# Optimization experiments

Measured on AMD Instinct MI355X. Metric: run time of the kernel, lower is better.

## Reference

```python
import jax, jax.numpy as jnp
import numpy as np

B, M, F_IN, DX, K, L, N_ALL = 8192, 10, 128, 128, 64, 32, 100000
NN = M - 1          # n_neigh
INF = float(M)


def layer_norm(x, g, b, eps=1e-5):
    mu = x.mean(-1, keepdims=True)
    var = ((x - mu) ** 2).mean(-1, keepdims=True)
    return (x - mu) * jax.lax.rsqrt(var + eps) * g + b


def bfs_dists(adj, mask):
    # normalized all-pairs hop distances via repeated boolean matmul (m=10 fixed)
    adj_bin = (adj > 1e-5).astype(jnp.float32)
    eye = jnp.eye(M, dtype=bool)
    d = jnp.where(eye[None], 0.0, jnp.where(adj_bin > 0, 1.0, INF))
    curr = adj_bin
    for k in range(2, M):
        curr = jnp.matmul(curr, adj_bin)
        d = jnp.where((curr > 0) & (d == INF), float(k), d)
    mask2 = mask[:, :, None] * mask[:, None, :]
    d = jnp.where(mask2 == 0, INF, d)
    return d / float(M)


def compute_sw(zb, zp, theta, vmask):
    # sliced Wasserstein-2 between batch point clouds [B,NN,d] and prototypes [K,NN,d]
    tn = theta / jnp.linalg.norm(theta, axis=1, keepdims=True)
    pb = jnp.einsum('bmd,ld->bml', zb, tn)
    pp = jnp.einsum('kmd,ld->kml', zp, tn)
    idx = jnp.argsort(pb, axis=1)
    pbs = jnp.take_along_axis(pb, idx, axis=1)
    pps = jnp.sort(pp, axis=1)
    w = jnp.take_along_axis(jnp.broadcast_to(vmask[:, :, None], pb.shape), idx, axis=1)
    w = w / (w.sum(axis=1, keepdims=True) + 1e-9)
    # sum_m w*(pb-pp)^2 expanded to avoid materializing [B,K,NN,L]
    t1 = (w * pbs ** 2).sum(axis=1)                   # [B,L]
    t2 = jnp.einsum('bml,kml->bkl', w * pbs, pps)     # [B,K,L]
    t3 = jnp.einsum('bml,kml->bkl', w, pps ** 2)
    return (t1[:, None, :] - 2.0 * t2 + t3).mean(axis=-1)


def compute_radial(rb, rp, vmask):
    idx = jnp.argsort(rb, axis=1)
    rbs = jnp.take_along_axis(rb, idx, axis=1)
    rps = jnp.sort(rp, axis=1)
    w = jnp.take_along_axis(vmask, idx, axis=1)
    w = w / (w.sum(axis=1, keepdims=True) + 1e-9)
    return (((rbs[:, None, :] - rps[None]) ** 2) * w[:, None, :]).sum(-1)


def setup_inputs() -> dict:
    key = jax.random.key(0)
    ks = jax.random.split(key, 16)
    up = (jax.random.uniform(ks[0], (B, M, M)) < 0.3).astype(jnp.float32)
    adj = jnp.maximum(up, up.transpose(0, 2, 1)) * (1.0 - jnp.eye(M))
    features = jax.random.normal(ks[1], (N_ALL, F_IN), jnp.float32)
    idxs = jax.random.randint(ks[2], (B, M), 0, N_ALL + 1)   # N_ALL == padding index
    rn = lambda k, s, sc=0.02: sc * jax.random.normal(k, s, jnp.float32)
    params = dict(
        x_lin_w=rn(ks[3], (F_IN, DX), 0.05), x_lin_b=jnp.zeros((DX,)),
        x_ln_g=jnp.ones((DX,)), x_ln_b=jnp.zeros((DX,)),
        s_ln_g=jnp.ones((NN,)), s_ln_b=jnp.zeros((NN,)),
        theta_x=jax.random.normal(ks[4], (L, DX), jnp.float32),
        theta_s=jax.random.normal(ks[5], (L, NN), jnp.float32),
        alpha_raw=jnp.zeros(()),
        an_w1=rn(ks[6], (DX, 32), 0.1), an_b1=jnp.zeros((32,)),
        an_w2=rn(ks[7], (32, 1), 0.1), an_b2=jnp.zeros((1,)),
        wn_w1=rn(ks[8], (2 * DX, 32), 0.1), wn_b1=jnp.zeros((32,)),
        wn_w2=rn(ks[9], (32, 1), 0.1), wn_b2=jnp.zeros((1,)),
        w_raw=jnp.zeros(()),
        proto_root=jax.random.normal(ks[10], (K, F_IN), jnp.float32),
        proto_neigh=jax.random.normal(ks[11], (K, NN, F_IN), jnp.float32),
        proto_rad=jax.random.uniform(ks[12], (K, NN)),
        proto_dn=jax.random.uniform(ks[13], (NN * (NN - 1) // 2, K), minval=-0.5, maxval=0.5),
        log_gamma=jnp.asarray(np.log(0.01), jnp.float32),
    )
    return {"adj": adj, "features": features, "idxs": idxs, **params}


def reference(adj, features, idxs, x_lin_w, x_lin_b, x_ln_g, x_ln_b, s_ln_g, s_ln_b,
              theta_x, theta_s, alpha_raw, an_w1, an_b1, an_w2, an_b2,
              wn_w1, wn_b1, wn_w2, wn_b2, w_raw,
              proto_root, proto_neigh, proto_rad, proto_dn, log_gamma):
    b = adj.shape[0]
    x_all = jnp.concatenate([features, jnp.zeros((1, F_IN), features.dtype)], 0)
    x_patch = x_all[idxs]                             # [B,M,F]
    x_root, x_neigh = x_patch[:, 0], x_patch[:, 1:]
    vmask = (idxs[:, 1:] != N_ALL).astype(jnp.float32)   # [B,NN]
    lin = lambda x: x @ x_lin_w + x_lin_b
    h_root = layer_norm(lin(x_root), x_ln_g, x_ln_b)
    h_proto_root = layer_norm(lin(proto_root), x_ln_g, x_ln_b)
    d_root_feat = (jnp.sum(h_root ** 2, -1)[:, None] + jnp.sum(h_proto_root ** 2, -1)[None]
                   - 2.0 * h_root @ h_proto_root.T)   # squared cdist [B,K]
    full_mask = jnp.concatenate([jnp.ones((b, 1), jnp.float32), vmask], 1)
    dists_full = bfs_dists(adj, full_mask)
    d_radial_str = compute_radial(dists_full[:, 0, 1:], proto_rad, vmask)
    h_neigh = layer_norm(lin(x_neigh), x_ln_g, x_ln_b)     # dropout = identity (eval)
    h_proto_neigh = layer_norm(lin(proto_neigh), x_ln_g, x_ln_b)
    sw_neigh_feat = compute_sw(h_neigh, h_proto_neigh, theta_x, vmask)
    hs_neigh = layer_norm(jnp.sort(dists_full[:, 1:, 1:], axis=1), s_ln_g, s_ln_b)
    ti, tj = np.triu_indices(NN, 1)
    C = jnp.zeros((K, NN, NN)).at[:, ti, tj].set(jax.nn.sigmoid(proto_dn).T)
    C = C + C.transpose(0, 2, 1)
    hs_proto = layer_norm(jnp.sort(C, axis=1), s_ln_g, s_ln_b)
    sw_neigh_str = compute_sw(hs_neigh, hs_proto, theta_s, vmask)
    h_pooled = (h_neigh * vmask[:, :, None]).sum(1) / (vmask.sum(1, keepdims=True) + 1e-9)
    alpha_logit = jnp.maximum(h_pooled @ an_w1 + an_b1, 0.0) @ an_w2 + an_b2   # [B,1]
    alpha = jax.nn.sigmoid(alpha_raw + alpha_logit)
    # pairwise w_net([h_root; h_proto_root]) without materializing [B,K,2*DX]
    hb = h_root @ wn_w1[:DX] + wn_b1                   # [B,32]
    hp = h_proto_root @ wn_w1[DX:]                     # [K,32]
    w_logit = (jnp.maximum(hb[:, None] + hp[None], 0.0) @ wn_w2)[..., 0] + wn_b2[0]
    w = jax.nn.sigmoid(w_raw + w_logit)                # [B,K]
    d_feat = w * d_root_feat + (1.0 - w) * sw_neigh_feat
    d_str = w * d_radial_str + (1.0 - w) * sw_neigh_str
    d_fgw = alpha * d_feat + (1.0 - alpha) * d_str
    return jnp.exp(-jnp.exp(log_gamma) * d_fgw)        # [B,K]
```

## Files before the change

### kernel.cpp

```cpp
#include <hip/hip_runtime.h>
#include <hip/hip_bf16.h>

typedef unsigned short u16;
typedef __attribute__((ext_vector_type(8))) short short8;
typedef __attribute__((ext_vector_type(4))) float f32x4;

#define NN 9
#define DX 128
#define KP 64
#define LL 32
#define NALL 100000
#define NBM 16
#define HXR 136
#define HXB (10 * HXR)

#define MFMA(a, b, c) __builtin_amdgcn_mfma_f32_16x16x32_bf16(a, b, c, 0, 0, 0)
#define WFENCE() __threadfence_block()

__device__ __align__(16) float g_tns[LL * NN];
__device__ __align__(16) float g_hprn[KP];
__device__ __align__(16) float g_hpt[32 * KP];
__device__ __align__(16) float g_rpst[NN * KP];
__device__ __align__(16) u16   g_pW[16384];
__device__ __align__(16) u16   g_pBt[4096];
__device__ __align__(16) u16   g_pBr[8192];
__device__ __align__(16) u16   g_pBx[36864];
__device__ __align__(16) u16   g_pBs[36864];
__device__ __align__(16) u16   g_pAn[4096];
__device__ __align__(16) u16   g_pWn[4096];

__device__ __forceinline__ float bf2f(u16 u) {
    union { unsigned u; float f; } v; v.u = ((unsigned)u) << 16; return v.f;
}
__device__ __forceinline__ u16 f2bf(float f) {
    __hip_bfloat16 h = __float2bfloat16(f);
    union { __hip_bfloat16 h; u16 u; } v; v.h = h; return v.u;
}
__device__ __forceinline__ float ldv(const void* p, long i, int f32) {
    return f32 ? ((const float*)p)[i] : bf2f(((const u16*)p)[i]);
}
__device__ __forceinline__ float sigmoidf(float x) { return 1.f / (1.f + expf(-x)); }

__device__ __forceinline__ int bfrag_idx(int ksteps, int ncol, int kd) {
    int ntile = ncol >> 4, n = ncol & 15;
    int kstep = kd >> 5, quad = (kd >> 3) & 3, j = kd & 7;
    return ((ntile * ksteps + kstep) * 64 + quad * 16 + n) * 8 + j;
}

__device__ __forceinline__ void rank9(const float* v, int* r) {
#pragma unroll
    for (int m = 0; m < 9; m++) {
        int rk = 0;
#pragma unroll
        for (int n = 0; n < 9; n++)
            rk += (v[n] < v[m]) || (v[n] == v[m] && n < m);
        r[m] = rk;
    }
}

__global__ __launch_bounds__(256) void k_pack(
    const void* xlw, const void* theta_x, const void* theta_s,
    const void* an_w1, const void* wn_w1, const void* xlg) {
    int t = threadIdx.x;
    const int f32 = (((const u16*)xlg)[0] == 0);
    if (blockIdx.x == 0) {
        for (int i = t; i < 16384; i += 256) {
            int c = i >> 7, d = i & 127;
            g_pW[bfrag_idx(4, d, c)] = f2bf(ldv(xlw, i, f32));
        }
    } else if (blockIdx.x == 1) {
        if (t < 32) {
            float s = 0;
            for (int d = 0; d < 128; d++) { float v = ldv(theta_x, t * 128 + d, f32); s = fmaf(v, v, s); }
            float inv = 1.f / sqrtf(s);
            for (int d = 0; d < 128; d++)
                g_pBt[bfrag_idx(4, t, d)] = f2bf(ldv(theta_x, t * 128 + d, f32) * inv);
        } else if (t < 64) {
            int l = t - 32;
            float s = 0;
            for (int j = 0; j < 9; j++) { float v = ldv(theta_s, l * 9 + j, f32); s = fmaf(v, v, s); }
            float inv = 1.f / sqrtf(s);
            for (int j = 0; j < 9; j++) g_tns[l * 9 + j] = ldv(theta_s, l * 9 + j, f32) * inv;
        }
    } else {
        for (int i = t; i < 4096; i += 256) {
            int d = i >> 5, j = i & 31;
            g_pAn[bfrag_idx(4, j, d)] = f2bf(ldv(an_w1, i, f32));
            g_pWn[bfrag_idx(4, j, d)] = f2bf(ldv(wn_w1, i, f32));
        }
    }
}

__global__ __launch_bounds__(256, 4) void k_proto(
    const void* proto_root, const void* proto_neigh,
    const void* xlb, const void* xlg, const void* xlbt,
    const void* slg, const void* slb, const void* wn_w1,
    const void* proto_rad, const void* proto_dn) {
    __shared__ __align__(16) u16   WfL[16384];
    __shared__ __align__(16) u16   hXpb[1280];
    __shared__ __align__(16) float pbX[288];
    __shared__ __align__(16) float Cm[84];
    __shared__ __align__(16) float hsnP[84];

    int t = threadIdx.x, lane = t & 63, w = t >> 6;
    const int f32 = (((const u16*)xlg)[0] == 0);
    int fm = lane & 15, quad = lane >> 4;
    int kb = blockIdx.x;

    {
        const short8* src = (const short8*)g_pW;
        short8* dst = (short8*)WfL;
#pragma unroll
        for (int i = 0; i < 8; i++) dst[t + 256 * i] = src[t + 256 * i];
    }

    int lr = w * 16 + fm;
    const void* abuf = proto_root; long aoff = 0;
    bool arow = (lr < 10);
    if (arow) {
        if (lr < 9) { abuf = proto_neigh; aoff = (long)(kb * 9 + lr) * 128; }
        else        { abuf = proto_root;  aoff = (long)kb * 128; }
    }
    short8 af[4];
#pragma unroll
    for (int ks = 0; ks < 4; ks++) af[ks] = (short8){0, 0, 0, 0, 0, 0, 0, 0};
    if (arow) {
        if (f32) {
#pragma unroll
            for (int ks = 0; ks < 4; ks++) {
                const f32x4* src = (const f32x4*)((const float*)abuf + aoff + ks * 32 + quad * 8);
                f32x4 v0 = src[0], v1 = src[1];
                u16* ap = (u16*)&af[ks];
#pragma unroll
                for (int j = 0; j < 4; j++) { ap[j] = f2bf(v0[j]); ap[4 + j] = f2bf(v1[j]); }
            }
        } else {
#pragma unroll
            for (int ks = 0; ks < 4; ks++)
                af[ks] = *(const short8*)((const u16*)abuf + aoff + ks * 32 + quad * 8);
        }
    }
    float bias8[8], gg8[8], bb8[8];
#pragma unroll
    for (int nt = 0; nt < 8; nt++) {
        int col = nt * 16 + fm;
        bias8[nt] = ldv(xlb, col, f32);
        gg8[nt]   = ldv(xlg, col, f32);
        bb8[nt]   = ldv(xlbt, col, f32);
    }
    __syncthreads();

    if (w == 0) {
        f32x4 acc[8];
#pragma unroll
        for (int nt = 0; nt < 8; nt++) acc[nt] = (f32x4){0.f, 0.f, 0.f, 0.f};
#pragma unroll
        for (int ks = 0; ks < 4; ks++) {
#pragma unroll
            for (int nt = 0; nt < 8; nt++) {
                short8 bf = *(const short8*)(WfL + ((nt * 4 + ks) * 64 + lane) * 8);
                acc[nt] = MFMA(af[ks], bf, acc[nt]);
            }
        }
#pragma unroll
        for (int reg = 0; reg < 4; reg++) {
            float s = 0, q = 0;
#pragma unroll
            for (int nt = 0; nt < 8; nt++) {
                float v = acc[nt][reg] + bias8[nt];
                s += v; q = fmaf(v, v, q);
            }
#pragma unroll
            for (int m = 1; m < 16; m <<= 1) { s += __shfl_xor(s, m); q += __shfl_xor(q, m); }
            float mu = s * (1.f / 128.f);
            float var = fmaxf(q * (1.f / 128.f) - mu * mu, 0.f);
            float rs = rsqrtf(var + 1e-5f);
            int rowD = quad * 4 + reg;
            if (rowD < 10) {
#pragma unroll
                for (int nt = 0; nt < 8; nt++) {
                    float val = (acc[nt][reg] + bias8[nt] - mu) * rs * gg8[nt] + bb8[nt];
                    hXpb[rowD * 128 + nt * 16 + fm] = f2bf(val);
                }
            }
        }
    }
    __syncthreads();

    for (int i = t; i < 128; i += 256)
        g_pBr[bfrag_idx(4, kb, i)] = hXpb[1152 + i];
    if (w == 0) {
        float v0 = bf2f(hXpb[1152 + lane]);
        float v1 = bf2f(hXpb[1216 + lane]);
        float q = v0 * v0 + v1 * v1;
#pragma unroll
        for (int m = 32; m >= 1; m >>= 1) q += __shfl_xor(q, m);
        if (lane == 0) g_hprn[kb] = q;
    }
    {
        int j = t >> 3, sub = t & 7;
        float a = 0;
#pragma unroll
        for (int dd = 0; dd < 16; dd++) {
            int d = sub * 16 + dd;
            a = fmaf(bf2f(hXpb[1152 + d]), ldv(wn_w1, (128 + d) * 32 + j, f32), a);
        }
        a += __shfl_xor(a, 1);
        a += __shfl_xor(a, 2);
        a += __shfl_xor(a, 4);
        if (sub == 0) g_hpt[j * 64 + kb] = a;
    }
    if (t == 0) {
        float v[9]; int r[9];
#pragma unroll
        for (int m = 0; m < 9; m++) v[m] = ldv(proto_rad, kb * 9 + m, f32);
        rank9(v, r);
#pragma unroll
        for (int m = 0; m < 9; m++) g_rpst[r[m] * 64 + kb] = v[m];
    }
    if (w == 0) {
        f32x4 acc0 = {0.f, 0.f, 0.f, 0.f}, acc1 = {0.f, 0.f, 0.f, 0.f};
        const u16* arow2 = hXpb + fm * 128;
#pragma unroll
        for (int ks = 0; ks < 4; ks++) {
            short8 afp = {0, 0, 0, 0, 0, 0, 0, 0};
            if (fm < 9) afp = *(const short8*)(arow2 + ks * 32 + quad * 8);
            short8 b0 = *(const short8*)(g_pBt + ((0 * 4 + ks) * 64 + lane) * 8);
            short8 b1 = *(const short8*)(g_pBt + ((1 * 4 + ks) * 64 + lane) * 8);
            acc0 = MFMA(afp, b0, acc0);
            acc1 = MFMA(afp, b1, acc1);
        }
#pragma unroll
        for (int reg = 0; reg < 4; reg++) {
            int row = quad * 4 + reg;
            if (row < 9) {
                pbX[row * 32 + fm]      = acc0[reg];
                pbX[row * 32 + 16 + fm] = acc1[reg];
            }
        }
    }
    for (int i = t; i < 81; i += 256) {
        int ii = i / 9, jj = i % 9; float v = 0.f;
        if (ii != jj) {
            int a = (ii < jj) ? ii : jj, b2 = (ii < jj) ? jj : ii;
            int p = a * 8 - a * (a - 1) / 2 + (b2 - a - 1);
            v = sigmoidf(ldv(proto_dn, p * 64 + kb, f32));
        }
        Cm[i] = v;
    }
    __syncthreads();
    if (t < 32) {
// ... 30 lines not shown
        float rs = rsqrtf(var + 1e-5f);
#pragma unroll
        for (int j = 0; j < 9; j++)
            hsnP[t * 9 + j] = (Cm[t * 9 + j] - mu) * rs * ldv(slg, j, f32) + ldv(slb, j, f32);
    }
    __syncthreads();
    if (t < 32) {
#pragma unroll
        for (int m = 0; m < 9; m++) {
            float a = 0;
#pragma unroll
            for (int j = 0; j < 9; j++) a = fmaf(hsnP[m * 9 + j], g_tns[t * 9 + j], a);
            pbX[m * 32 + t] = a;
        }
    }
    __syncthreads();
    if (t < 32) {
        float v[9]; int r[9];
#pragma unroll
        for (int m = 0; m < 9; m++) v[m] = pbX[m * 32 + t];
        rank9(v, r);
#pragma unroll
        for (int m = 0; m < 9; m++) {
            int kd = t * 9 + r[m];
            g_pBs[bfrag_idx(18, kb, kd)]       = f2bf(v[m] * v[m]);
            g_pBs[bfrag_idx(18, kb, 288 + kd)] = f2bf(v[m]);
        }
    }
}

struct M3 {
    u16   Cf[NBM][584];
    u16   Cs[NBM][584];
    u16   hpoolb[NBM][136];
    u16   hX[NBM][HXB];
    float pb[NBM][288];
    float df[NBM][100];
    float hst[NBM][81];
    float drad[NBM][65];
    float hbv[NBM][33];
    float rbss[NBM][9], wrad[NBM][9];
    float sc[NBM][9];
};
__global__ __launch_bounds__(1024, 4) void k_main(
    const void* adj, const void* feat, const int* idxs,
    const void* slg, const void* slb,
    const void* xlb, const void* xlg, const void* xlbt,
    const void* an_b1, const void* an_w2, const void* an_b2,
    const void* wn_b1, const void* wn_w2, const void* wn_b2,
    const void* alpha_raw, const void* w_raw, const void* log_gamma,
    void* out, int B) {
    __shared__ __align__(16) M3 S;
    int t = threadIdx.x, lane = t & 63, w = t >> 6;
    const int f32 = (((const u16*)xlg)[0] == 0);
    int fm = lane & 15, quad = lane >> 4;
    int bw = blockIdx.x * NBM + w;
    bool bv = (bw < B);

    unsigned long long mb = 0; float nv = 1e-9f, inv = 0.f;

    if (bv) {
        bool azero = true; long aoff = 0;
        if (fm < 10) {
            int id = idxs[bw * 10 + fm];
            if (id != NALL) { azero = false; aoff = (long)id * 128; }
        }
        short8 af[4];
#pragma unroll
        for (int ks = 0; ks < 4; ks++) af[ks] = (short8){0, 0, 0, 0, 0, 0, 0, 0};
        if (!azero) {
            if (f32) {
#pragma unroll
                for (int ks = 0; ks < 4; ks++) {
                    const f32x4* src = (const f32x4*)((const float*)feat + aoff + ks * 32 + quad * 8);
                    f32x4 v0 = src[0], v1 = src[1];
                    u16* ap = (u16*)&af[ks];
#pragma unroll
                    for (int j = 0; j < 4; j++) { ap[j] = f2bf(v0[j]); ap[4 + j] = f2bf(v1[j]); }
                }
            } else {
#pragma unroll
                for (int ks = 0; ks < 4; ks++)
                    af[ks] = *(const short8*)((const u16*)feat + aoff + ks * 32 + quad * 8);
            }
        }

        bool valid = false;
        if (lane < 10) {
            int id = idxs[bw * 10 + lane];
            valid = (lane == 0) || (id != NALL);
        }
        mb = __ballot(valid);
        nv = (float)__popcll(mb & 0x3FEull) + 1e-9f;
        inv = 1.f / nv;
        unsigned rowbits = 0;
        if (lane < 10) {
            for (int j = 0; j < 10; j++)
                if (ldv(adj, (long)bw * 100 + lane * 10 + j, f32) > 1e-5f) rowbits |= 1u << j;
        }
        int dl[10];
#pragma unroll
        for (int j = 0; j < 10; j++) dl[j] = (j == lane) ? 0 : (((rowbits >> j) & 1) ? 1 : 10);
        unsigned reach = (lane < 10) ? (rowbits | (1u << lane)) : 0u;
        for (int s = 2; s <= 9; s++) {
            unsigned nr = reach;
#pragma unroll
            for (int j = 0; j < 10; j++) {
                unsigned rj = __shfl(rowbits, j);
                if ((reach >> j) & 1) nr |= rj;
            }
            unsigned add = nr & ~reach;
#pragma unroll
            for (int j = 0; j < 10; j++) if ((add >> j) & 1) dl[j] = s;
            reach = nr;
            if (__all(add == 0)) break;
        }
        if (lane < 10) {
            int mi = (int)((mb >> lane) & 1);
#pragma unroll
            for (int j = 0; j < 10; j++) {
                int mj = (int)((mb >> j) & 1);
                S.df[w][lane * 10 + j] = (mi && mj) ? (float)dl[j] * 0.1f : 1.0f;
            }
        }
        {
            float v[9];
#pragma unroll
            for (int m = 0; m < 9; m++) {
                float vm = ((mb >> (1 + m)) & 1) ? (float)dl[1 + m] * 0.1f : 1.0f;
                v[m] = __shfl(vm, 0);
            }
            if (lane < 9) {
                float mine = v[0];
#pragma unroll
                for (int m = 1; m < 9; m++) if (lane == m) mine = v[m];
                int rk = 0;
#pragma unroll
                for (int n = 0; n < 9; n++) rk += (v[n] < mine) || (v[n] == mine && n < lane);
                S.rbss[w][rk] = mine;
                S.wrad[w][rk] = (((mb >> (1 + lane)) & 1) ? 1.f : 0.f) * inv;
            }
        }

        {
            float bias8[8], gg8[8], bb8[8];
#pragma unroll
            for (int nt = 0; nt < 8; nt++) {
                int col = nt * 16 + fm;
                bias8[nt] = ldv(xlb, col, f32);
                gg8[nt]   = ldv(xlg, col, f32);
                bb8[nt]   = ldv(xlbt, col, f32);
            }
            f32x4 acc[8];
#pragma unroll
            for (int nt = 0; nt < 8; nt++) acc[nt] = (f32x4){0.f, 0.f, 0.f, 0.f};
#pragma unroll
            for (int ks = 0; ks < 4; ks++) {
#pragma unroll
                for (int nt = 0; nt < 8; nt++) {
                    short8 bf = *(const short8*)(g_pW + ((nt * 4 + ks) * 64 + lane) * 8);
                    acc[nt] = MFMA(af[ks], bf, acc[nt]);
                }
            }
#pragma unroll
            for (int reg = 0; reg < 4; reg++) {
                float s = 0, q = 0;
#pragma unroll
                for (int nt = 0; nt < 8; nt++) {
                    float v = acc[nt][reg] + bias8[nt];
                    s += v; q = fmaf(v, v, q);
                }
#pragma unroll
                for (int m = 1; m < 16; m <<= 1) { s += __shfl_xor(s, m); q += __shfl_xor(q, m); }
                float mu = s * (1.f / 128.f);
                float var = fmaxf(q * (1.f / 128.f) - mu * mu, 0.f);
                float rs = rsqrtf(var + 1e-5f);
                int rowD = quad * 4 + reg;
                if (rowD < 10) {
#pragma unroll
                    for (int nt = 0; nt < 8; nt++) {
                        float val = (acc[nt][reg] + bias8[nt] - mu) * rs * gg8[nt] + bb8[nt];
                        S.hX[w][rowD * HXR + nt * 16 + fm] = f2bf(val);
                    }
                }
            }
        }
        WFENCE();

        {
            float v0 = bf2f(S.hX[w][lane]), v1 = bf2f(S.hX[w][64 + lane]);
            float q = v0 * v0 + v1 * v1;
#pragma unroll
            for (int m = 32; m >= 1; m >>= 1) q += __shfl_xor(q, m);
            if (lane == 0) S.sc[w][1] = q;
        }
        for (int dd = lane; dd < 128; dd += 64) {
            float a = 0;
#pragma unroll
            for (int m = 0; m < 9; m++) {
                float hv = bf2f(S.hX[w][(1 + m) * HXR + dd]);
                float msk = ((mb >> (1 + m)) & 1) ? 1.f : 0.f;
                a = fmaf(hv, msk, a);
            }
            S.hpoolb[w][dd] = f2bf(a * inv);
        }
        {
            f32x4 acc0 = {0.f, 0.f, 0.f, 0.f}, acc1 = {0.f, 0.f, 0.f, 0.f};
            const u16* arow = S.hX[w] + (1 + fm) * HXR;
#pragma unroll
            for (int ks = 0; ks < 4; ks++) {
                short8 afn = {0, 0, 0, 0, 0, 0, 0, 0};
                if (fm < 9) afn = *(const short8*)(arow + ks * 32 + quad * 8);
                short8 b0 = *(const short8*)(g_pBt + ((0 * 4 + ks) * 64 + lane) * 8);
                short8 b1 = *(const short8*)(g_pBt + ((1 * 4 + ks) * 64 + lane) * 8);
                acc0 = MFMA(afn, b0, acc0);
                acc1 = MFMA(afn, b1, acc1);
            }
#pragma unroll
            for (int reg = 0; reg < 4; reg++) {
                int row = quad * 4 + reg;
                if (row < 9) {
                    S.pb[w][row * 32 + fm]      = acc0[reg];
                    S.pb[w][row * 32 + 16 + fm] = acc1[reg];
                }
            }
        }
        WFENCE();

        {
            float t1 = 0;
            if (lane < 32) {
                float v[9]; int r[9];
#pragma unroll
                for (int m = 0; m < 9; m++) v[m] = S.pb[w][m * 32 + lane];
                rank9(v, r);
#pragma unroll
                for (int m = 0; m < 9; m++) {
                    float wgt = (((mb >> (1 + m)) & 1) ? 1.f : 0.f) * inv;
                    int slot = lane * 9 + r[m];
                    S.Cf[w][slot]       = f2bf(wgt);
                    S.Cf[w][288 + slot] = f2bf(-2.f * wgt * v[m]);
                    t1 = fmaf(wgt * v[m], v[m], t1);
                }
            }
#pragma unroll
            for (int m = 16; m >= 1; m >>= 1) t1 += __shfl_xor(t1, m);
            if (lane == 0) S.sc[w][3] = t1;
        }
        if (lane < 9) {
            float v[9]; int r[9];
#pragma unroll
            for (int i = 0; i < 9; i++) v[i] = S.df[w][(1 + i) * 10 + 1 + lane];
            rank9(v, r);
#pragma unroll
            for (int i = 0; i < 9; i++) S.hst[w][r[i] * 9 + lane] = v[i];
        }
        {
            float acc = 0;
#pragma unroll
            for (int m = 0; m < 9; m++) {
                float d0 = S.rbss[w][m] - g_rpst[m * 64 + lane];
                acc = fmaf(d0 * d0, S.wrad[w][m], acc);
            }
            S.drad[w][lane] = acc;
        }
        WFENCE();

        if (lane < 9) {
            float vv[9];
#pragma unroll
            for (int j = 0; j < 9; j++) vv[j] = S.hst[w][lane * 9 + j];
            float mu = 0;
#pragma unroll
            for (int j = 0; j < 9; j++) mu += vv[j];
            mu *= (1.f / 9.f);
            float var = 0;
#pragma unroll
            for (int j = 0; j < 9; j++) { float d0 = vv[j] - mu; var = fmaf(d0, d0, var); }
            var *= (1.f / 9.f);
            float rs = rsqrtf(var + 1e-5f);
#pragma unroll
            for (int j = 0; j < 9; j++)
                S.hst[w][lane * 9 + j] = (vv[j] - mu) * rs * ldv(slg, j, f32) + ldv(slb, j, f32);
        }
        WFENCE();

        {
            int l = lane & 31;
            int m0 = (lane < 32) ? 0 : 5, m1 = (lane < 32) ? 5 : 9;
            for (int m = m0; m < m1; m++) {
                float a = 0;
#pragma unroll
                for (int j = 0; j < 9; j++) a = fmaf(S.hst[w][m * 9 + j], g_tns[l * 9 + j], a);
                S.pb[w][m * 32 + l] = a;
            }
        }
        WFENCE();

        {
            float t1 = 0;
            if (lane < 32) {
                float v[9]; int r[9];
#pragma unroll
                for (int m = 0; m < 9; m++) v[m] = S.pb[w][m * 32 + lane];
                rank9(v, r);
#pragma unroll
                for (int m = 0; m < 9; m++) {
                    float wgt = (((mb >> (1 + m)) & 1) ? 1.f : 0.f) * inv;
                    int slot = lane * 9 + r[m];
                    S.Cs[w][slot]       = f2bf(wgt);
                    S.Cs[w][288 + slot] = f2bf(-2.f * wgt * v[m]);
                    t1 = fmaf(wgt * v[m], v[m], t1);
                }
            }
#pragma unroll
            for (int m = 16; m >= 1; m >>= 1) t1 += __shfl_xor(t1, m);
            if (lane == 0) S.sc[w][4] = t1;
        }
    }
    __syncthreads();

    f32x4 rd = {0.f, 0.f, 0.f, 0.f};
    f32x4 accF = {0.f, 0.f, 0.f, 0.f}, accS = {0.f, 0.f, 0.f, 0.f};
    if (w < 4) {
#pragma unroll
        for (int ks = 0; ks < 4; ks++) {
            short8 af = {0, 0, 0, 0, 0, 0, 0, 0};
            if (blockIdx.x * NBM + fm < B)
                af = *(const short8*)(S.hX[fm] + ks * 32 + quad * 8);
            short8 bfr = *(const short8*)(g_pBr + ((w * 4 + ks) * 64 + lane) * 8);
            rd = MFMA(af, bfr, rd);
        }
#pragma unroll
        for (int ks = 0; ks < 18; ks++) {
            short8 aF = *(const short8*)(S.Cf[fm] + ks * 32 + quad * 8);
            short8 aS = *(const short8*)(S.Cs[fm] + ks * 32 + quad * 8);
            short8 bF = *(const short8*)(g_pBx + ((w * 18 + ks) * 64 + lane) * 8);
            short8 bS = *(const short8*)(g_pBs + ((w * 18 + ks) * 64 + lane) * 8);
            accF = MFMA(aF, bF, accF);
            accS = MFMA(aS, bS, accS);
        }
    } else if (w == 4) {
        f32x4 a0 = {0.f, 0.f, 0.f, 0.f}, a1 = {0.f, 0.f, 0.f, 0.f};
#pragma unroll
        for (int ks = 0; ks < 4; ks++) {
            short8 af = {0, 0, 0, 0, 0, 0, 0, 0};
            if (blockIdx.x * NBM + fm < B)
                af = *(const short8*)(S.hX[fm] + ks * 32 + quad * 8);
            short8 b0 = *(const short8*)(g_pWn + ((0 * 4 + ks) * 64 + lane) * 8);
            short8 b1 = *(const short8*)(g_pWn + ((1 * 4 + ks) * 64 + lane) * 8);
            a0 = MFMA(af, b0, a0);
            a1 = MFMA(af, b1, a1);
        }
        float wb0 = ldv(wn_b1, fm, f32), wb1 = ldv(wn_b1, 16 + fm, f32);
#pragma unroll
        for (int reg = 0; reg < 4; reg++) {
            int b = quad * 4 + reg;
            S.hbv[b][fm]      = a0[reg] + wb0;
            S.hbv[b][16 + fm] = a1[reg] + wb1;
        }
    } else if (w == 5) {
        f32x4 a0 = {0.f, 0.f, 0.f, 0.f}, a1 = {0.f, 0.f, 0.f, 0.f};
#pragma unroll
        for (int ks = 0; ks < 4; ks++) {
            short8 af = *(const short8*)(S.hpoolb[fm] + ks * 32 + quad * 8);
            short8 b0 = *(const short8*)(g_pAn + ((0 * 4 + ks) * 64 + lane) * 8);
            short8 b1 = *(const short8*)(g_pAn + ((1 * 4 + ks) * 64 + lane) * 8);
            a0 = MFMA(af, b0, a0);
            a1 = MFMA(af, b1, a1);
        }
        float ab0 = ldv(an_b1, fm, f32), ab1 = ldv(an_b1, 16 + fm, f32);
        float aw0 = ldv(an_w2, fm, f32), aw1 = ldv(an_w2, 16 + fm, f32);
        float araw = ldv(alpha_raw, 0, f32), ab2 = ldv(an_b2, 0, f32);
#pragma unroll
        for (int reg = 0; reg < 4; reg++) {
            float s = fmaxf(a0[reg] + ab0, 0.f) * aw0 + fmaxf(a1[reg] + ab1, 0.f) * aw1;
            s += __shfl_xor(s, 1); s += __shfl_xor(s, 2);
            s += __shfl_xor(s, 4); s += __shfl_xor(s, 8);
            if (fm == 0) S.sc[quad * 4 + reg][2] = sigmoidf(araw + s + ab2);
        }
    }
// ... 34 lines not shown
    }
}

extern "C" void kernel_launch(void* const* d_in, const int* in_sizes, int n_in,
                              void* d_out, int out_size, void* d_ws, size_t ws_size,
                              hipStream_t stream) {
    const void* adj  = d_in[0];
    const void* feat = d_in[1];
    const int*  idxs = (const int*)d_in[2];
    const void* xlw  = d_in[3];
    const void* xlb  = d_in[4];
    const void* xlg  = d_in[5];
    const void* xlbt = d_in[6];
    const void* slg  = d_in[7];
    const void* slb  = d_in[8];
    const void* thx  = d_in[9];
    const void* ths  = d_in[10];
    const void* araw = d_in[11];
    const void* anw1 = d_in[12];
    const void* anb1 = d_in[13];
    const void* anw2 = d_in[14];
    const void* anb2 = d_in[15];
    const void* wnw1 = d_in[16];
    const void* wnb1 = d_in[17];
    const void* wnw2 = d_in[18];
    const void* wnb2 = d_in[19];
    const void* wraw = d_in[20];
    const void* prt  = d_in[21];
    const void* prn  = d_in[22];
    const void* prad = d_in[23];
    const void* pdn  = d_in[24];
    const void* lgam = d_in[25];
    int B = in_sizes[2] / 10;

    k_pack<<<3, 256, 0, stream>>>(xlw, thx, ths, anw1, wnw1, xlg);
    k_proto<<<KP, 256, 0, stream>>>(prt, prn, xlb, xlg, xlbt, slg, slb, wnw1,
                                    prad, pdn);
    k_main<<<(B + NBM - 1) / NBM, 1024, 0, stream>>>(adj, feat, idxs, slg, slb,
                                  xlb, xlg, xlbt,
                                  anb1, anw2, anb2, wnb1, wnw2, wnb2,
                                  araw, wraw, lgam, d_out, B);
}
```

Baseline: 226.8 us.

## Split per-sample preprocessing into separate kernel merged with prototype blocks

Moves the per-sample work (feature gather, linear+layernorm, BFS distances, projections, sorting, radial distances) out of the 1024-thread main kernel into a new 256-thread kernel with one wave per sample. The new kernel shares its grid with the prototype blocks. Results are staged through global scratch buffers, which the main kernel then loads into shared memory before its MFMA distance stage. This aims for higher occupancy and overlap of the serial per-sample work with prototype processing. The cost is extra global traffic for the intermediate buffers and reading the weight fragments from global instead of LDS.

```diff
diff --git a/kernel.cpp b/kernel.cpp
--- a/kernel.cpp
+++ b/kernel.cpp
@@ -10,9 +10,11 @@
 #define KP 64
 #define LL 32
 #define NALL 100000
+#define BMAX 8192
 #define NBM 16
+#define NBP 64
 #define HXR 136
-#define HXB (10 * HXR)
+#define WSTR 4736
 
 #define MFMA(a, b, c) __builtin_amdgcn_mfma_f32_16x16x32_bf16(a, b, c, 0, 0, 0)
 #define WFENCE() __threadfence_block()
@@ -21,6 +23,14 @@
 __device__ __align__(16) float g_hprn[KP];
 __device__ __align__(16) float g_hpt[32 * KP];
 __device__ __align__(16) float g_rpst[NN * KP];
+__device__ __align__(16) u16   g_hroot[BMAX * DX];
+__device__ __align__(16) u16   g_hpool[BMAX * DX];
+__device__ __align__(16) float g_hrn[BMAX];
+__device__ __align__(16) u16   g_Cf[BMAX * 576];
+__device__ __align__(16) u16   g_Cs[BMAX * 576];
+__device__ __align__(16) float g_drad[BMAX * 64];
+__device__ __align__(16) float g_t1x[BMAX];
+__device__ __align__(16) float g_t1s[BMAX];
 __device__ __align__(16) u16   g_pW[16384];
 __device__ __align__(16) u16   g_pBt[4096];
 __device__ __align__(16) u16   g_pBr[8192];
@@ -60,7 +70,7 @@
 
 __global__ __launch_bounds__(256) void k_pack(
     const void* xlw, const void* theta_x, const void* theta_s,
-    const void* an_w1, const void* wn_w1, const void* xlg) {
+    const void* an_w1, const void* wn_w1, const void* proto_rad, const void* xlg) {
     int t = threadIdx.x;
     const int f32 = (((const u16*)xlg)[0] == 0);
     if (blockIdx.x == 0) {
@@ -81,6 +91,14 @@
             for (int j = 0; j < 9; j++) { float v = ldv(theta_s, l * 9 + j, f32); s = fmaf(v, v, s); }
             float inv = 1.f / sqrtf(s);
             for (int j = 0; j < 9; j++) g_tns[l * 9 + j] = ldv(theta_s, l * 9 + j, f32) * inv;
+        } else if (t < 128) {
+            int k = t - 64;
+            float v[9]; int r[9];
+#pragma unroll
+            for (int m = 0; m < 9; m++) v[m] = ldv(proto_rad, k * 9 + m, f32);
+            rank9(v, r);
+#pragma unroll
+            for (int m = 0; m < 9; m++) g_rpst[r[m] * 64 + k] = v[m];
         }
     } else {
         for (int i = t; i < 4096; i += 256) {
@@ -91,66 +109,330 @@
     }
 }
 
-__global__ __launch_bounds__(256, 4) void k_proto(
+__global__ __launch_bounds__(256, 5) void k_lin(
+    const void* adj, const void* feat, const int* idxs,
     const void* proto_root, const void* proto_neigh,
     const void* xlb, const void* xlg, const void* xlbt,
     const void* slg, const void* slb, const void* wn_w1,
-    const void* proto_rad, const void* proto_dn) {
-    __shared__ __align__(16) u16   WfL[16384];
-    __shared__ __align__(16) u16   hXpb[1280];
-    __shared__ __align__(16) float pbX[288];
-    __shared__ __align__(16) float Cm[84];
-    __shared__ __align__(16) float hsnP[84];
+    const void* proto_dn, int B) {
+    __shared__ __align__(16) char sm[4 * WSTR];
 
     int t = threadIdx.x, lane = t & 63, w = t >> 6;
     const int f32 = (((const u16*)xlg)[0] == 0);
     int fm = lane & 15, quad = lane >> 4;
+    bool isProto = (blockIdx.x < (unsigned)NBP);
+
+    if (!isProto) {
+        u16*   hSw = (u16*)(sm + w * WSTR);
+        float* pbw = (float*)(sm + w * WSTR + 2720);
+        float* dfw = (float*)(sm + w * WSTR + 3872);
+        float* stw = (float*)(sm + w * WSTR + 4272);
+        float* rbw = (float*)(sm + w * WSTR + 4608);
+        float* wrw = (float*)(sm + w * WSTR + 4644);
+
+        int bw = (blockIdx.x - NBP) * 4 + w;
+        if (bw >= B) return;
+
+        bool valid = false;
+        if (lane < 10) {
+            int id = idxs[bw * 10 + lane];
+            valid = (lane == 0) || (id != NALL);
+        }
+        unsigned long long mb = __ballot(valid);
+        float inv = 1.f / ((float)__popcll(mb & 0x3FEull) + 1e-9f);
+
+        bool azero = true; long aoff = 0;
+        if (fm < 10) {
+            int id2 = idxs[bw * 10 + fm];
+            if (id2 != NALL) { azero = false; aoff = (long)id2 * 128; }
+        }
+        short8 af[4];
+#pragma unroll
+        for (int ks = 0; ks < 4; ks++) af[ks] = (short8){0, 0, 0, 0, 0, 0, 0, 0};
+        if (!azero) {
+            if (f32) {
+#pragma unroll
+                for (int ks = 0; ks < 4; ks++) {
+                    const f32x4* src = (const f32x4*)((const float*)feat + aoff + ks * 32 + quad * 8);
+                    f32x4 v0 = src[0], v1 = src[1];
+                    u16* ap = (u16*)&af[ks];
+#pragma unroll
+                    for (int j = 0; j < 4; j++) { ap[j] = f2bf(v0[j]); ap[4 + j] = f2bf(v1[j]); }
+                }
+            } else {
+#pragma unroll
+                for (int ks = 0; ks < 4; ks++)
+                    af[ks] = *(const short8*)((const u16*)feat + aoff + ks * 32 + quad * 8);
+            }
+        }
+
+        unsigned rowbits = 0;
+        if (lane < 10) {
+            for (int j = 0; j < 10; j++)
+                if (ldv(adj, (long)bw * 100 + lane * 10 + j, f32) > 1e-5f) rowbits |= 1u << j;
+        }
+        int dl[10];
+#pragma unroll
+        for (int j = 0; j < 10; j++) dl[j] = (j == lane) ? 0 : (((rowbits >> j) & 1) ? 1 : 10);
+        unsigned reach = (lane < 10) ? (rowbits | (1u << lane)) : 0u;
+        for (int s = 2; s <= 9; s++) {
+            unsigned nr = reach;
+#pragma unroll
+            for (int j = 0; j < 10; j++) {
+                unsigned rj = __shfl(rowbits, j);
+                if ((reach >> j) & 1) nr |= rj;
+            }
+            unsigned add = nr & ~reach;
+#pragma unroll
+            for (int j = 0; j < 10; j++) if ((add >> j) & 1) dl[j] = s;
+            reach = nr;
+            if (__all(add == 0)) break;
+        }
+        if (lane < 10) {
+            int mi = (int)((mb >> lane) & 1);
+#pragma unroll
+            for (int j = 0; j < 10; j++) {
+                int mj = (int)((mb >> j) & 1);
+                dfw[lane * 10 + j] = (mi && mj) ? (float)dl[j] * 0.1f : 1.0f;
+            }
+        }
+        {
+            float v[9];
+#pragma unroll
+            for (int m = 0; m < 9; m++) {
+                float vm = ((mb >> (1 + m)) & 1) ? (float)dl[1 + m] * 0.1f : 1.0f;
+                v[m] = __shfl(vm, 0);
+            }
+            if (lane < 9) {
+                float mine = v[0];
+#pragma unroll
+                for (int m = 1; m < 9; m++) if (lane == m) mine = v[m];
+                int rk = 0;
+#pragma unroll
+                for (int n = 0; n < 9; n++) rk += (v[n] < mine) || (v[n] == mine && n < lane);
+                rbw[rk] = mine;
+                wrw[rk] = (((mb >> (1 + lane)) & 1) ? 1.f : 0.f) * inv;
+            }
+        }
+
+        {
+            float bias8[8], gg8[8], bb8[8];
+#pragma unroll
+            for (int nt = 0; nt < 8; nt++) {
+                int col = nt * 16 + fm;
+                bias8[nt] = ldv(xlb, col, f32);
+                gg8[nt]   = ldv(xlg, col, f32);
+                bb8[nt]   = ldv(xlbt, col, f32);
+            }
+            f32x4 acc[8];
+#pragma unroll
+            for (int nt = 0; nt < 8; nt++) acc[nt] = (f32x4){0.f, 0.f, 0.f, 0.f};
+#pragma unroll
+            for (int ks = 0; ks < 4; ks++) {
+#pragma unroll
+                for (int nt = 0; nt < 8; nt++) {
+                    short8 bf = *(const short8*)(g_pW + ((nt * 4 + ks) * 64 + lane) * 8);
+                    acc[nt] = MFMA(af[ks], bf, acc[nt]);
+                }
+            }
+#pragma unroll
+            for (int reg = 0; reg < 4; reg++) {
+                float s = 0, q = 0;
+#pragma unroll
+                for (int nt = 0; nt < 8; nt++) {
+                    float v = acc[nt][reg] + bias8[nt];
+                    s += v; q = fmaf(v, v, q);
+                }
+#pragma unroll
+                for (int m = 1; m < 16; m <<= 1) { s += __shfl_xor(s, m); q += __shfl_xor(q, m); }
+                float mu = s * (1.f / 128.f);
+                float var = fmaxf(q * (1.f / 128.f) - mu * mu, 0.f);
+                float rs = rsqrtf(var + 1e-5f);
+                int rowD = quad * 4 + reg;
+                if (rowD < 10) {
+#pragma unroll
+                    for (int nt = 0; nt < 8; nt++) {
+                        float val = (acc[nt][reg] + bias8[nt] - mu) * rs * gg8[nt] + bb8[nt];
+                        hSw[rowD * HXR + nt * 16 + fm] = f2bf(val);
+                    }
+                }
+            }
+        }
+        WFENCE();
+
+        if (lane < 16)
+            ((short8*)(g_hroot + (long)bw * 128))[lane] = ((const short8*)hSw)[lane];
+        {
+            float v0 = bf2f(hSw[lane]), v1 = bf2f(hSw[64 + lane]);
+            float q = v0 * v0 + v1 * v1;
+#pragma unroll
+            for (int m = 32; m >= 1; m >>= 1) q += __shfl_xor(q, m);
+            if (lane == 0) g_hrn[bw] = q;
+        }
+        {
+            float a0 = 0, a1 = 0;
+            int c0 = lane * 2, c1 = lane * 2 + 1;
+#pragma unroll
+            for (int m = 0; m < 9; m++) {
+                float msk = ((mb >> (1 + m)) & 1) ? 1.f : 0.f;
+                a0 = fmaf(bf2f(hSw[(1 + m) * HXR + c0]), msk, a0);
+                a1 = fmaf(bf2f(hSw[(1 + m) * HXR + c1]), msk, a1);
+            }
+            unsigned pk = (unsigned)f2bf(a0 * inv) | ((unsigned)f2bf(a1 * inv) << 16);
+            ((unsigned*)(g_hpool + (long)bw * 128))[lane] = pk;
+        }
+
+        {
+            f32x4 acc0 = {0.f, 0.f, 0.f, 0.f}, acc1 = {0.f, 0.f, 0.f, 0.f};
+            const u16* arow = hSw + (1 + fm) * HXR;
+#pragma unroll
+            for (int ks = 0; ks < 4; ks++) {
+                short8 afn = {0, 0, 0, 0, 0, 0, 0, 0};
+                if (fm < 9) afn = *(const short8*)(arow + ks * 32 + quad * 8);
+                short8 b0 = *(const short8*)(g_pBt + ((0 * 4 + ks) * 64 + lane) * 8);
+                short8 b1 = *(const short8*)(g_pBt + ((1 * 4 + ks) * 64 + lane) * 8);
+                acc0 = MFMA(afn, b0, acc0);
+                acc1 = MFMA(afn, b1, acc1);
+            }
+#pragma unroll
+            for (int reg = 0; reg < 4; reg++) {
+                int row = quad * 4 + reg;
+                if (row < 9) {
+                    pbw[row * 32 + fm]      = acc0[reg];
+                    pbw[row * 32 + 16 + fm] = acc1[reg];
+                }
+            }
+        }
+        WFENCE();
+
+        {
+            float t1 = 0;
+            if (lane < 32) {
+                float v[9]; int r[9];
+#pragma unroll
+                for (int m = 0; m < 9; m++) v[m] = pbw[m * 32 + lane];
+                rank9(v, r);
+#pragma unroll
+                for (int m = 0; m < 9; m++) {
+                    float wgt = (((mb >> (1 + m)) & 1) ? 1.f : 0.f) * inv;
+                    int slot = lane * 9 + r[m];
+                    g_Cf[(long)bw * 576 + slot]       = f2bf(wgt);
+                    g_Cf[(long)bw * 576 + 288 + slot] = f2bf(-2.f * wgt * v[m]);
+                    t1 = fmaf(wgt * v[m], v[m], t1);
+                }
+            }
+#pragma unroll
+            for (int m = 16; m >= 1; m >>= 1) t1 += __shfl_xor(t1, m);
+            if (lane == 0) g_t1x[bw] = t1;
+        }
+        if (lane < 9) {
+            float v[9]; int r[9];
+#pragma unroll
+            for (int i = 0; i < 9; i++) v[i] = dfw[(1 + i) * 10 + 1 + lane];
+            rank9(v, r);
+#pragma unroll
+            for (int i = 0; i < 9; i++) stw[r[i] * 9 + lane] = v[i];
+        }
+        WFENCE();
+        if (lane < 9) {
+            float vv[9];
+#pragma unroll
+            for (int j = 0; j < 9; j++) vv[j] = stw[lane * 9 + j];
+            float mu = 0;
+#pragma unroll
+            for (int j = 0; j < 9; j++) mu += vv[j];
+            mu *= (1.f / 9.f);
+            float var = 0;
+#pragma unroll
+            for (int j = 0; j < 9; j++) { float d0 = vv[j] - mu; var = fmaf(d0, d0, var); }
+            var *= (1.f / 9.f);
+            float rs = rsqrtf(var + 1e-5f);
+#pragma unroll
+            for (int j = 0; j < 9; j++)
+                stw[lane * 9 + j] = (vv[j] - mu) * rs * ldv(slg, j, f32) + ldv(slb, j, f32);
+        }
+        WFENCE();
+        {
+            int l = lane & 31;
+            int m0 = (lane < 32) ? 0 : 5, m1 = (lane < 32) ? 5 : 9;
+            for (int m = m0; m < m1; m++) {
+                float a = 0;
+#pragma unroll
+                for (int j = 0; j < 9; j++) a = fmaf(stw[m * 9 + j], g_tns[l * 9 + j], a);
+                pbw[m * 32 + l] = a;
+            }
+        }
+        WFENCE();
+        {
+            float t1 = 0;
+            if (lane < 32) {
+                float v[9]; int r[9];
+#pragma unroll
+                for (int m = 0; m < 9; m++) v[m] = pbw[m * 32 + lane];
+                rank9(v, r);
+#pragma unroll
+                for (int m = 0; m < 9; m++) {
+                    float wgt = (((mb >> (1 + m)) & 1) ? 1.f : 0.f) * inv;
+                    int slot = lane * 9 + r[m];
+                    g_Cs[(long)bw * 576 + slot]       = f2bf(wgt);
+                    g_Cs[(long)bw * 576 + 288 + slot] = f2bf(-2.f * wgt * v[m]);
+                    t1 = fmaf(wgt * v[m], v[m], t1);
+                }
+            }
+#pragma unroll
+            for (int m = 16; m >= 1; m >>= 1) t1 += __shfl_xor(t1, m);
+            if (lane == 0) g_t1s[bw] = t1;
+        }
+        {
+            float a = 0;
+#pragma unroll
+            for (int m = 0; m < 9; m++) {
+                float d0 = rbw[m] - g_rpst[m * 64 + lane];
+                a = fmaf(d0 * d0, wrw[m], a);
+            }
+            g_drad[(long)bw * 64 + lane] = a;
+        }
+        return;
+    }
+
+    u16*   hXpb = (u16*)sm;
+    float* pbX  = (float*)(sm + 2560);
+    float* Cm   = (float*)(sm + 3712);
+    float* hsnP = (float*)(sm + 4048);
     int kb = blockIdx.x;
 
-    {
-        const short8* src = (const short8*)g_pW;
-        short8* dst = (short8*)WfL;
-#pragma unroll
-        for (int i = 0; i < 8; i++) dst[t + 256 * i] = src[t + 256 * i];
-    }
-
-    int lr = w * 16 + fm;
-    const void* abuf = proto_root; long aoff = 0;
-    bool arow = (lr < 10);
-    if (arow) {
-        if (lr < 9) { abuf = proto_neigh; aoff = (long)(kb * 9 + lr) * 128; }
+    if (w == 0) {
+        const void* abuf; long aoff;
+        if (fm < 9) { abuf = proto_neigh; aoff = (long)(kb * 9 + fm) * 128; }
         else        { abuf = proto_root;  aoff = (long)kb * 128; }
-    }
-    short8 af[4];
-#pragma unroll
-    for (int ks = 0; ks < 4; ks++) af[ks] = (short8){0, 0, 0, 0, 0, 0, 0, 0};
-    if (arow) {
-        if (f32) {
-#pragma unroll
-            for (int ks = 0; ks < 4; ks++) {
-                const f32x4* src = (const f32x4*)((const float*)abuf + aoff + ks * 32 + quad * 8);
-                f32x4 v0 = src[0], v1 = src[1];
-                u16* ap = (u16*)&af[ks];
-#pragma unroll
-                for (int j = 0; j < 4; j++) { ap[j] = f2bf(v0[j]); ap[4 + j] = f2bf(v1[j]); }
-            }
-        } else {
-#pragma unroll
-            for (int ks = 0; ks < 4; ks++)
-                af[ks] = *(const short8*)((const u16*)abuf + aoff + ks * 32 + quad * 8);
-        }
-    }
-    float bias8[8], gg8[8], bb8[8];
-#pragma unroll
-    for (int nt = 0; nt < 8; nt++) {
-        int col = nt * 16 + fm;
-        bias8[nt] = ldv(xlb, col, f32);
-        gg8[nt]   = ldv(xlg, col, f32);
-        bb8[nt]   = ldv(xlbt, col, f32);
-    }
-    __syncthreads();
-
-    if (w == 0) {
+        bool arow = (fm < 10);
+        short8 af[4];
+#pragma unroll
+        for (int ks = 0; ks < 4; ks++) af[ks] = (short8){0, 0, 0, 0, 0, 0, 0, 0};
+        if (arow) {
+            if (f32) {
+#pragma unroll
+                for (int ks = 0; ks < 4; ks++) {
+                    const f32x4* src = (const f32x4*)((const float*)abuf + aoff + ks * 32 + quad * 8);
+                    f32x4 v0 = src[0], v1 = src[1];
+                    u16* ap = (u16*)&af[ks];
+#pragma unroll
+                    for (int j = 0; j < 4; j++) { ap[j] = f2bf(v0[j]); ap[4 + j] = f2bf(v1[j]); }
+                }
+            } else {
+#pragma unroll
+                for (int ks = 0; ks < 4; ks++)
+                    af[ks] = *(const short8*)((const u16*)abuf + aoff + ks * 32 + quad * 8);
+            }
+        }
+        float bias8[8], gg8[8], bb8[8];
+#pragma unroll
+        for (int nt = 0; nt < 8; nt++) {
+            int col = nt * 16 + fm;
+            bias8[nt] = ldv(xlb, col, f32);
+            gg8[nt]   = ldv(xlg, col, f32);
+            bb8[nt]   = ldv(xlbt, col, f32);
+        }
         f32x4 acc[8];
 #pragma unroll
         for (int nt = 0; nt < 8; nt++) acc[nt] = (f32x4){0.f, 0.f, 0.f, 0.f};
@@ -158,7 +440,7 @@
         for (int ks = 0; ks < 4; ks++) {
 #pragma unroll
             for (int nt = 0; nt < 8; nt++) {
-                short8 bf = *(const short8*)(WfL + ((nt * 4 + ks) * 64 + lane) * 8);
+                short8 bf = *(const short8*)(g_pW + ((nt * 4 + ks) * 64 + lane) * 8);
                 acc[nt] = MFMA(af[ks], bf, acc[nt]);
             }
         }
@@ -209,14 +491,6 @@
         a += __shfl_xor(a, 2);
         a += __shfl_xor(a, 4);
         if (sub == 0) g_hpt[j * 64 + kb] = a;
-    }
-    if (t == 0) {
-        float v[9]; int r[9];
-#pragma unroll
-        for (int m = 0; m < 9; m++) v[m] = ldv(proto_rad, kb * 9 + m, f32);
-        rank9(v, r);
-#pragma unroll
-        for (int m = 0; m < 9; m++) g_rpst[r[m] * 64 + kb] = v[m];
     }
     if (w == 0) {
         f32x4 acc0 = {0.f, 0.f, 0.f, 0.f}, acc1 = {0.f, 0.f, 0.f, 0.f};
@@ -313,24 +587,17 @@
 struct M3 {
     u16   Cf[NBM][584];
     u16   Cs[NBM][584];
+    u16   hrootL[NBM][136];
     u16   hpoolb[NBM][136];
-    u16   hX[NBM][HXB];
-    float pb[NBM][288];
-    float df[NBM][100];
-    float hst[NBM][81];
     float drad[NBM][65];
     float hbv[NBM][33];
-    float rbss[NBM][9], wrad[NBM][9];
     float sc[NBM][9];
 };
-__global__ __launch_bounds__(1024, 4) void k_main(
-    const void* adj, const void* feat, const int* idxs,
-    const void* slg, const void* slb,
-    const void* xlb, const void* xlg, const void* xlbt,
+__global__ __launch_bounds__(1024, 8) void k_main(
     const void* an_b1, const void* an_w2, const void* an_b2,
     const void* wn_b1, const void* wn_w2, const void* wn_b2,
     const void* alpha_raw, const void* w_raw, const void* log_gamma,
-    void* out, int B) {
+    const void* xlg, void* out, int B) {
     __shared__ __align__(16) M3 S;
     int t = threadIdx.x, lane = t & 63, w = t >> 6;
     const int f32 = (((const u16*)xlg)[0] == 0);
@@ -338,265 +605,36 @@
     int bw = blockIdx.x * NBM + w;
     bool bv = (bw < B);
 
-    unsigned long long mb = 0; float nv = 1e-9f, inv = 0.f;
-
     if (bv) {
-        bool azero = true; long aoff = 0;
-        if (fm < 10) {
-            int id = idxs[bw * 10 + fm];
-            if (id != NALL) { azero = false; aoff = (long)id * 128; }
-        }
-        short8 af[4];
-#pragma unroll
-        for (int ks = 0; ks < 4; ks++) af[ks] = (short8){0, 0, 0, 0, 0, 0, 0, 0};
-        if (!azero) {
-            if (f32) {
-#pragma unroll
-                for (int ks = 0; ks < 4; ks++) {
-                    const f32x4* src = (const f32x4*)((const float*)feat + aoff + ks * 32 + quad * 8);
-                    f32x4 v0 = src[0], v1 = src[1];
-                    u16* ap = (u16*)&af[ks];
-#pragma unroll
-                    for (int j = 0; j < 4; j++) { ap[j] = f2bf(v0[j]); ap[4 + j] = f2bf(v1[j]); }
-                }
-            } else {
-#pragma unroll
-                for (int ks = 0; ks < 4; ks++)
-                    af[ks] = *(const short8*)((const u16*)feat + aoff + ks * 32 + quad * 8);
-            }
-        }
-
-        bool valid = false;
-        if (lane < 10) {
-            int id = idxs[bw * 10 + lane];
-            valid = (lane == 0) || (id != NALL);
-        }
-        mb = __ballot(valid);
-        nv = (float)__popcll(mb & 0x3FEull) + 1e-9f;
-        inv = 1.f / nv;
-        unsigned rowbits = 0;
-        if (lane < 10) {
-            for (int j = 0; j < 10; j++)
-                if (ldv(adj, (long)bw * 100 + lane * 10 + j, f32) > 1e-5f) rowbits |= 1u << j;
-        }
-        int dl[10];
-#pragma unroll
-        for (int j = 0; j < 10; j++) dl[j] = (j == lane) ? 0 : (((rowbits >> j) & 1) ? 1 : 10);
-        unsigned reach = (lane < 10) ? (rowbits | (1u << lane)) : 0u;
-        for (int s = 2; s <= 9; s++) {
-            unsigned nr = reach;
-#pragma unroll
-            for (int j = 0; j < 10; j++) {
-                unsigned rj = __shfl(rowbits, j);
-                if ((reach >> j) & 1) nr |= rj;
-            }
-            unsigned add = nr & ~reach;
-#pragma unroll
-            for (int j = 0; j < 10; j++) if ((add >> j) & 1) dl[j] = s;
-            reach = nr;
-            if (__all(add == 0)) break;
-        }
-        if (lane < 10) {
-            int mi = (int)((mb >> lane) & 1);
-#pragma unroll
-            for (int j = 0; j < 10; j++) {
-                int mj = (int)((mb >> j) & 1);
-                S.df[w][lane * 10 + j] = (mi && mj) ? (float)dl[j] * 0.1f : 1.0f;
-            }
-        }
-        {
-            float v[9];
-#pragma unroll
-            for (int m = 0; m < 9; m++) {
-                float vm = ((mb >> (1 + m)) & 1) ? (float)dl[1 + m] * 0.1f : 1.0f;
-                v[m] = __shfl(vm, 0);
-            }
-            if (lane < 9) {
-                float mine = v[0];
-#pragma unroll
-                for (int m = 1; m < 9; m++) if (lane == m) mine = v[m];
-                int rk = 0;
-#pragma unroll
-                for (int n = 0; n < 9; n++) rk += (v[n] < mine) || (v[n] == mine && n < lane);
-                S.rbss[w][rk] = mine;
-                S.wrad[w][rk] = (((mb >> (1 + lane)) & 1) ? 1.f : 0.f) * inv;
-            }
-        }
-
-        {
-            float bias8[8], gg8[8], bb8[8];
-#pragma unroll
-            for (int nt = 0; nt < 8; nt++) {
-                int col = nt * 16 + fm;
-                bias8[nt] = ldv(xlb, col, f32);
-                gg8[nt]   = ldv(xlg, col, f32);
-                bb8[nt]   = ldv(xlbt, col, f32);
-            }
-            f32x4 acc[8];
-#pragma unroll
-            for (int nt = 0; nt < 8; nt++) acc[nt] = (f32x4){0.f, 0.f, 0.f, 0.f};
-#pragma unroll
-            for (int ks = 0; ks < 4; ks++) {
-#pragma unroll
-                for (int nt = 0; nt < 8; nt++) {
-                    short8 bf = *(const short8*)(g_pW + ((nt * 4 + ks) * 64 + lane) * 8);
-                    acc[nt] = MFMA(af[ks], bf, acc[nt]);
-                }
-            }
-#pragma unroll
-            for (int reg = 0; reg < 4; reg++) {
-                float s = 0, q = 0;
-#pragma unroll
-                for (int nt = 0; nt < 8; nt++) {
-                    float v = acc[nt][reg] + bias8[nt];
-                    s += v; q = fmaf(v, v, q);
-                }
-#pragma unroll
-                for (int m = 1; m < 16; m <<= 1) { s += __shfl_xor(s, m); q += __shfl_xor(q, m); }
-                float mu = s * (1.f / 128.f);
-                float var = fmaxf(q * (1.f / 128.f) - mu * mu, 0.f);
-                float rs = rsqrtf(var + 1e-5f);
-                int rowD = quad * 4 + reg;
-                if (rowD < 10) {
-#pragma unroll
-                    for (int nt = 0; nt < 8; nt++) {
-                        float val = (acc[nt][reg] + bias8[nt] - mu) * rs * gg8[nt] + bb8[nt];
-                        S.hX[w][rowD * HXR + nt * 16 + fm] = f2bf(val);
-                    }
-                }
-            }
-        }
-        WFENCE();
-
-        {
-            float v0 = bf2f(S.hX[w][lane]), v1 = bf2f(S.hX[w][64 + lane]);
-            float q = v0 * v0 + v1 * v1;
-#pragma unroll
-            for (int m = 32; m >= 1; m >>= 1) q += __shfl_xor(q, m);
-            if (lane == 0) S.sc[w][1] = q;
-        }
-        for (int dd = lane; dd < 128; dd += 64) {
-            float a = 0;
-#pragma unroll
-            for (int m = 0; m < 9; m++) {
-                float hv = bf2f(S.hX[w][(1 + m) * HXR + dd]);
-                float msk = ((mb >> (1 + m)) & 1) ? 1.f : 0.f;
-                a = fmaf(hv, msk, a);
-            }
-            S.hpoolb[w][dd] = f2bf(a * inv);
-        }
-        {
-            f32x4 acc0 = {0.f, 0.f, 0.f, 0.f}, acc1 = {0.f, 0.f, 0.f, 0.f};
-            const u16* arow = S.hX[w] + (1 + fm) * HXR;
-#pragma unroll
-            for (int ks = 0; ks < 4; ks++) {
-                short8 afn = {0, 0, 0, 0, 0, 0, 0, 0};
-                if (fm < 9) afn = *(const short8*)(arow + ks * 32 + quad * 8);
-                short8 b0 = *(const short8*)(g_pBt + ((0 * 4 + ks) * 64 + lane) * 8);
-                short8 b1 = *(const short8*)(g_pBt + ((1 * 4 + ks) * 64 + lane) * 8);
-                acc0 = MFMA(afn, b0, acc0);
-                acc1 = MFMA(afn, b1, acc1);
-            }
-#pragma unroll
-            for (int reg = 0; reg < 4; reg++) {
-                int row = quad * 4 + reg;
-                if (row < 9) {
-                    S.pb[w][row * 32 + fm]      = acc0[reg];
-                    S.pb[w][row * 32 + 16 + fm] = acc1[reg];
-                }
-            }
-        }
-        WFENCE();
-
-        {
-            float t1 = 0;
-            if (lane < 32) {
-                float v[9]; int r[9];
-#pragma unroll
-                for (int m = 0; m < 9; m++) v[m] = S.pb[w][m * 32 + lane];
-                rank9(v, r);
-#pragma unroll
-                for (int m = 0; m < 9; m++) {
-                    float wgt = (((mb >> (1 + m)) & 1) ? 1.f : 0.f) * inv;
-                    int slot = lane * 9 + r[m];
-                    S.Cf[w][slot]       = f2bf(wgt);
-                    S.Cf[w][288 + slot] = f2bf(-2.f * wgt * v[m]);
-                    t1 = fmaf(wgt * v[m], v[m], t1);
-                }
-            }
-#pragma unroll
-            for (int m = 16; m >= 1; m >>= 1) t1 += __shfl_xor(t1, m);
-            if (lane == 0) S.sc[w][3] = t1;
-        }
-        if (lane < 9) {
-            float v[9]; int r[9];
-#pragma unroll
-            for (int i = 0; i < 9; i++) v[i] = S.df[w][(1 + i) * 10 + 1 + lane];
-            rank9(v, r);
-#pragma unroll
-            for (int i = 0; i < 9; i++) S.hst[w][r[i] * 9 + lane] = v[i];
-        }
-        {
-            float acc = 0;
-#pragma unroll
-            for (int m = 0; m < 9; m++) {
-                float d0 = S.rbss[w][m] - g_rpst[m * 64 + lane];
-                acc = fmaf(d0 * d0, S.wrad[w][m], acc);
-            }
-            S.drad[w][lane] = acc;
-        }
-        WFENCE();
-
-        if (lane < 9) {
-            float vv[9];
-#pragma unroll
-            for (int j = 0; j < 9; j++) vv[j] = S.hst[w][lane * 9 + j];
-            float mu = 0;
-#pragma unroll
-            for (int j = 0; j < 9; j++) mu += vv[j];
-            mu *= (1.f / 9.f);
-            float var = 0;
-#pragma unroll
-            for (int j = 0; j < 9; j++) { float d0 = vv[j] - mu; var = fmaf(d0, d0, var); }
-            var *= (1.f / 9.f);
-            float rs = rsqrtf(var + 1e-5f);
-#pragma unroll
-            for (int j = 0; j < 9; j++)
-                S.hst[w][lane * 9 + j] = (vv[j] - mu) * rs * ldv(slg, j, f32) + ldv(slb, j, f32);
-        }
-        WFENCE();
-
-        {
-            int l = lane & 31;
-            int m0 = (lane < 32) ? 0 : 5, m1 = (lane < 32) ? 5 : 9;
-            for (int m = m0; m < m1; m++) {
-                float a = 0;
-#pragma unroll
-                for (int j = 0; j < 9; j++) a = fmaf(S.hst[w][m * 9 + j], g_tns[l * 9 + j], a);
-                S.pb[w][m * 32 + l] = a;
-            }
-        }
-        WFENCE();
-
-        {
-            float t1 = 0;
-            if (lane < 32) {
-                float v[9]; int r[9];
-#pragma unroll
-                for (int m = 0; m < 9; m++) v[m] = S.pb[w][m * 32 + lane];
-                rank9(v, r);
-#pragma unroll
-                for (int m = 0; m < 9; m++) {
-                    float wgt = (((mb >> (1 + m)) & 1) ? 1.f : 0.f) * inv;
-                    int slot = lane * 9 + r[m];
-                    S.Cs[w][slot]       = f2bf(wgt);
-                    S.Cs[w][288 + slot] = f2bf(-2.f * wgt * v[m]);
-                    t1 = fmaf(wgt * v[m], v[m], t1);
-                }
-            }
-#pragma unroll
-            for (int m = 16; m >= 1; m >>= 1) t1 += __shfl_xor(t1, m);
-            if (lane == 0) S.sc[w][4] = t1;
+        {
+            const short8* src = (const short8*)(g_Cf + (long)bw * 576);
+            short8* dst = (short8*)S.Cf[w];
+            for (int i = lane; i < 72; i += 64) dst[i] = src[i];
+        }
+        {
+            const short8* src = (const short8*)(g_Cs + (long)bw * 576);
+            short8* dst = (short8*)S.Cs[w];
+            for (int i = lane; i < 72; i += 64) dst[i] = src[i];
+        }
+        if (lane < 16) {
+            ((short8*)S.hrootL[w])[lane] = ((const short8*)(g_hroot + (long)bw * 128))[lane];
+            ((short8*)S.hpoolb[w])[lane] = ((const short8*)(g_hpool + (long)bw * 128))[lane];
+        }
+        S.drad[w][lane] = g_drad[(long)bw * 64 + lane];
+        if (lane == 0) {
+            S.sc[w][1] = g_hrn[bw];
+            S.sc[w][3] = g_t1x[bw];
+            S.sc[w][4] = g_t1s[bw];
+        }
+    } else {
+        short8 z = {0, 0, 0, 0, 0, 0, 0, 0};
+        for (int i = lane; i < 72; i += 64) {
+            ((short8*)S.Cf[w])[i] = z;
+            ((short8*)S.Cs[w])[i] = z;
+        }
+        if (lane < 16) {
+            ((short8*)S.hrootL[w])[lane] = z;
+            ((short8*)S.hpoolb[w])[lane] = z;
         }
     }
     __syncthreads();
@@ -606,9 +644,7 @@
     if (w < 4) {
 #pragma unroll
         for (int ks = 0; ks < 4; ks++) {
-            short8 af = {0, 0, 0, 0, 0, 0, 0, 0};
-            if (blockIdx.x * NBM + fm < B)
-                af = *(const short8*)(S.hX[fm] + ks * 32 + quad * 8);
+            short8 af = *(const short8*)(S.hrootL[fm] + ks * 32 + quad * 8);
             short8 bfr = *(const short8*)(g_pBr + ((w * 4 + ks) * 64 + lane) * 8);
             rd = MFMA(af, bfr, rd);
         }
@@ -625,9 +661,7 @@
         f32x4 a0 = {0.f, 0.f, 0.f, 0.f}, a1 = {0.f, 0.f, 0.f, 0.f};
 #pragma unroll
         for (int ks = 0; ks < 4; ks++) {
-            short8 af = {0, 0, 0, 0, 0, 0, 0, 0};
-            if (blockIdx.x * NBM + fm < B)
-                af = *(const short8*)(S.hX[fm] + ks * 32 + quad * 8);
+            short8 af = *(const short8*)(S.hrootL[fm] + ks * 32 + quad * 8);
             short8 b0 = *(const short8*)(g_pWn + ((0 * 4 + ks) * 64 + lane) * 8);
             short8 b1 = *(const short8*)(g_pWn + ((1 * 4 + ks) * 64 + lane) * 8);
             a0 = MFMA(af, b0, a0);
@@ -728,12 +762,13 @@
     const void* pdn  = d_in[24];
     const void* lgam = d_in[25];
     int B = in_sizes[2] / 10;
-
-    k_pack<<<3, 256, 0, stream>>>(xlw, thx, ths, anw1, wnw1, xlg);
-    k_proto<<<KP, 256, 0, stream>>>(prt, prn, xlb, xlg, xlbt, slg, slb, wnw1,
-                                    prad, pdn);
-    k_main<<<(B + NBM - 1) / NBM, 1024, 0, stream>>>(adj, feat, idxs, slg, slb,
-                                  xlb, xlg, xlbt,
+    int NBW = (B + 3) / 4;
+
+    k_pack<<<3, 256, 0, stream>>>(xlw, thx, ths, anw1, wnw1, prad, xlg);
+    k_lin<<<NBP + NBW, 256, 0, stream>>>(adj, feat, idxs, prt, prn,
+                                         xlb, xlg, xlbt, slg, slb, wnw1,
+                                         pdn, B);
+    k_main<<<(B + NBM - 1) / NBM, 1024, 0, stream>>>(
                                   anb1, anw2, anb2, wnb1, wnw2, wnb2,
-                                  araw, wraw, lgam, d_out, B);
-}
+                                  araw, wraw, lgam, xlg, d_out, B);
+}
```

Result: faster. 215.0 us (-5.2%).
